# Performance work log

Measured on AMD Instinct MI355X. Metric: run time of the kernel, lower is better.

## Reference

```python
import jax, jax.numpy as jnp
import numpy as np

N1 = 64          # n1 (rows of matching matrix)
N2 = 64          # n2 (cols); N = n1*n2 association-graph nodes
N = N1 * N2
DENSITY = 0.15   # sparsity of affinity matrix K
CH = [64, 64, 64]
TAU = 0.05
SK_ITERS = 20


def _sinkhorn(s):
    # log-domain Sinkhorn, tau=0.05, 20 alternating row/col normalizations.
    # n1 == n2 here, so the dummy_row padding in the original is a no-op.
    log_s = s / TAU
    for i in range(SK_ITERS):
        log_s = log_s - jax.nn.logsumexp(log_s, axis=(1 if i % 2 == 0 else 0), keepdims=True)
    return jnp.exp(log_s)


def _lin(k, i, o, scale=0.1):
    kw, kb = jax.random.split(k)
    return (jax.random.normal(kw, (i, o), jnp.float32) * scale,
            jax.random.normal(kb, (o,), jnp.float32) * scale)


def setup_inputs() -> dict:
    key = jax.random.key(0)
    ks = jax.random.split(key, 16)
    mask = jax.random.uniform(ks[0], (N, N)) < DENSITY
    mask = mask | jnp.eye(N, dtype=bool)          # diag(K) supplies node features
    K = jnp.where(mask, jax.random.normal(ks[1], (N, N), jnp.float32), 0.0)
    # identical to torch: (K != 0).nonzero(as_tuple=False).t()
    edge_index = jnp.stack(jnp.nonzero(K)).astype(jnp.int32)
    inp = {"K": K, "edge_index": edge_index, "n1": N1, "n2": N2}
    dims_in = [1, CH[0], CH[1]]
    ki = 2
    for l in range(3):
        cw, cb = _lin(ks[ki], dims_in[l], CH[l]); ki += 1
        sw, sb = _lin(ks[ki], dims_in[l], CH[l]); ki += 1
        kw, kb = _lin(ks[ki], CH[l], 1); ki += 1
        inp.update({f"conv_w{l}": cw, f"conv_b{l}": cb,
                    f"self_w{l}": sw, f"self_b{l}": sb,
                    f"cls_w{l}": kw, f"cls_b{l}": kb})
    fw, fb = _lin(ks[ki], CH[2], 1)
    inp["fin_w"] = fw
    inp["fin_b"] = fb
    return inp


def _forward(K, edge_index, n1, n2, layer_params, fin_w, fin_b):
    n_nodes = n1 * n2
    src, dst = edge_index[0], edge_index[1]
    loop = jnp.arange(n_nodes, dtype=src.dtype)
    # PyG gcn_norm / add_remaining_self_loops: existing self-loop edges get
    # weight replaced (zeroed here, re-added with weight 1 below).
    w = jnp.concatenate([(src != dst).astype(K.dtype), jnp.ones((n_nodes,), K.dtype)])
    src_f = jnp.concatenate([src, loop])
    dst_f = jnp.concatenate([dst, loop])
    deg = jax.ops.segment_sum(w, dst_f, num_segments=n_nodes)
    dis = jnp.where(deg > 0, jax.lax.rsqrt(deg), 0.0)
    norm = dis[src_f] * w * dis[dst_f]                    # (E+N,)

    x = jnp.diag(K)[:, None]                              # (N, 1) node features
    for (cw, cb, sw, sb, kw, kb) in layer_params:
        xw = x @ cw                                       # (N, out)
        x_neigh = jax.ops.segment_sum(norm[:, None] * xw[src_f], dst_f,
                                      num_segments=n_nodes) + cb
        x_out = (x @ sw + sb) + x_neigh                   # self-loop + GCNConv
        sk = _sinkhorn((x_out @ kw + kb).reshape(n1, n2))
        x = x_out + sk.reshape(n_nodes, 1)                # broadcast over channels
    scores = x @ fin_w + fin_b                            # (N, 1)
    s = scores.reshape(n2, n1).T                          # (n1, n2)
    return _sinkhorn(s)


def reference(K, edge_index, n1, n2,
              conv_w0, conv_b0, self_w0, self_b0, cls_w0, cls_b0,
              conv_w1, conv_b1, self_w1, self_b1, cls_w1, cls_b1,
              conv_w2, conv_b2, self_w2, self_b2, cls_w2, cls_b2,
              fin_w, fin_b):
    layer_params = [(conv_w0, conv_b0, self_w0, self_b0, cls_w0, cls_b0),
                    (conv_w1, conv_b1, self_w1, self_b1, cls_w1, cls_b1),
                    (conv_w2, conv_b2, self_w2, self_b2, cls_w2, cls_b2)]
    return _forward(K, edge_index, n1, n2, layer_params, fin_w, fin_b)
```

## Files before the change

kernel.cpp:

```cpp
#include <hip/hip_runtime.h>
#include <hip/hip_bf16.h>
#include <cstdint>
#include <cstddef>

#define NN 4096

typedef float f32x4 __attribute__((ext_vector_type(4)));
typedef short s16x8 __attribute__((ext_vector_type(8)));

__global__ __launch_bounds__(256) void k_prep(const float* __restrict__ K,
                                              unsigned long long* __restrict__ maskT) {
  const int lane = threadIdx.x & 63;
  const int wv = threadIdx.x >> 6;
  const int d0 = blockIdx.x * 256 + lane * 4;
  const int sbase = blockIdx.y * 256 + wv * 64;
  const int chunk = blockIdx.y * 4 + wv;
  unsigned long long w0 = 0, w1 = 0, w2 = 0, w3 = 0;
#pragma unroll 8
  for (int i = 0; i < 64; ++i) {
    const float4 kv = *(const float4*)(K + (size_t)(sbase + i) * NN + d0);
    w0 |= ((unsigned long long)(kv.x != 0.0f)) << i;
    w1 |= ((unsigned long long)(kv.y != 0.0f)) << i;
    w2 |= ((unsigned long long)(kv.z != 0.0f)) << i;
    w3 |= ((unsigned long long)(kv.w != 0.0f)) << i;
  }
  unsigned long long* mp = maskT + (size_t)chunk * NN + d0;
  mp[0] = w0; mp[1] = w1; mp[2] = w2; mp[3] = w3;
}

__device__ __forceinline__ void sinkhorn_pots(const float* __restrict__ matR,
    const float* __restrict__ matC, float* __restrict__ potU, float* __restrict__ potV,
    float* __restrict__ pp, int tid) {
  const int l = tid & 63;
  const int w = tid >> 6;
  const int jb = w * 16;
  if (w == 0) potV[l] = 0.f;
  __syncthreads();
  for (int it = 0; it < 20; ++it) {
    const bool row = (it & 1) == 0;
    const float* src = row ? matR : matC;
    const float* pot = row ? potV : potU;
    f32x4 x0 = *(const f32x4*)&src[l * 68 + jb];
    f32x4 x1 = *(const f32x4*)&src[l * 68 + jb + 4];
    f32x4 x2 = *(const f32x4*)&src[l * 68 + jb + 8];
    f32x4 x3 = *(const f32x4*)&src[l * 68 + jb + 12];
    const f32x4 p0 = *(const f32x4*)&pot[jb];
    const f32x4 p1 = *(const f32x4*)&pot[jb + 4];
    const f32x4 p2 = *(const f32x4*)&pot[jb + 8];
    const f32x4 p3 = *(const f32x4*)&pot[jb + 12];
    x0 -= p0; x1 -= p1; x2 -= p2; x3 -= p3;
    f32x4 mA;
#pragma unroll
    for (int i = 0; i < 4; ++i)
      mA[i] = fmaxf(fmaxf(x0[i], x1[i]), fmaxf(x2[i], x3[i]));
    const float mx = fmaxf(fmaxf(mA[0], mA[1]), fmaxf(mA[2], mA[3]));
    float sm = 0.f;
#pragma unroll
    for (int i = 0; i < 4; ++i)
      sm += __expf(x0[i] - mx) + __expf(x1[i] - mx) +
            __expf(x2[i] - mx) + __expf(x3[i] - mx);
    pp[l * 12 + w] = mx;
    pp[l * 12 + 4 + w] = sm;
    __syncthreads();
    if (w == 0) {
      const f32x4 pm = *(const f32x4*)&pp[l * 12];
      const f32x4 ps = *(const f32x4*)&pp[l * 12 + 4];
      const float mM = fmaxf(fmaxf(pm[0], pm[1]), fmaxf(pm[2], pm[3]));
      const float ss = ps[0] * __expf(pm[0] - mM) + ps[1] * __expf(pm[1] - mM)
                     + ps[2] * __expf(pm[2] - mM) + ps[3] * __expf(pm[3] - mM);
      const float lse = mM + __logf(ss);
      (row ? potU : potV)[l] = lse;
    }
    __syncthreads();
  }
}

__global__ __launch_bounds__(256) void k_xform0(const float* __restrict__ K,
    const unsigned long long* __restrict__ maskT,
    const float* __restrict__ cw, const float* __restrict__ cb,
    const float* __restrict__ sw, const float* __restrict__ sb,
    float* __restrict__ disv,
    __hip_bfloat16* __restrict__ gHi, __hip_bfloat16* __restrict__ gLo,
    float* __restrict__ xselfT) {
  __shared__ float pdeg[4][64];
  const int lane = threadIdx.x & 63;
  const int wv = threadIdx.x >> 6;
  const int s = blockIdx.x * 64 + lane;
  unsigned cnt = 0;
#pragma unroll
  for (int q = 0; q < 16; ++q)
    cnt += (unsigned)__popcll(maskT[(size_t)(wv * 16 + q) * NN + s]);
  pdeg[wv][lane] = (float)cnt;
  __syncthreads();
  const float ds = rsqrtf(pdeg[0][lane] + pdeg[1][lane] + pdeg[2][lane] + pdeg[3][lane]);
  if (wv == 0) disv[s] = ds;
  const float xv = K[(size_t)s * NN + s];
#pragma unroll
  for (int i = 0; i < 16; ++i) {
    const int c = wv * 16 + i;
    const float gv = ds * xv * cw[c];
    const __hip_bfloat16 hi = __float2bfloat16(gv);
    gHi[(size_t)c * NN + s] = hi;
    gLo[(size_t)c * NN + s] = __float2bfloat16(gv - __bfloat162float(hi));
    xselfT[(size_t)c * NN + s] = xv * sw[c] + sb[c] + cb[c];
  }
}

__global__ __launch_bounds__(256, 1) void k_xform(const float* __restrict__ v,
    const float* __restrict__ vT,
    const float* __restrict__ xoutT, const float* __restrict__ disv,
    const float* __restrict__ cw, const float* __restrict__ cb,
    const float* __restrict__ sw, const float* __restrict__ sb,
    __hip_bfloat16* __restrict__ gHi, __hip_bfloat16* __restrict__ gLo,
    float* __restrict__ xselfT) {
  __shared__ __align__(16) float matR[64 * 68];
  __shared__ __align__(16) float matC[64 * 68];
  __shared__ float xt[64][64];
  __shared__ float wcl[64 * 32], wsl[64 * 32];
  __shared__ __align__(16) float potU[64], potV[64], pp[64 * 12];
  const int tid = threadIdx.x;
  const int l = tid & 63;
  const int w = tid >> 6;
  const int jb = w * 16;
  const int s = blockIdx.x * 64 + l;
  const int cbase = blockIdx.y * 32;
#pragma unroll
  for (int q = 0; q < 4; ++q) {
    *(f32x4*)&matR[l * 68 + jb + 4 * q] = *(const f32x4*)&v[l * 64 + jb + 4 * q] * 20.0f;
    *(f32x4*)&matC[l * 68 + jb + 4 * q] = *(const f32x4*)&vT[l * 64 + jb + 4 * q] * 20.0f;
  }
#pragma unroll
  for (int r = 0; r < 16; ++r)
    xt[w * 16 + r][l] = xoutT[(size_t)(w * 16 + r) * NN + s];
#pragma unroll
  for (int q = 0; q < 8; ++q) {
    const int e = w * 512 + q * 64 + l;
    const int k = e >> 5, cl = e & 31;
    wcl[e] = cw[k * 64 + cbase + cl];
    wsl[e] = sw[k * 64 + cbase + cl];
  }
  sinkhorn_pots(matR, matC, potU, potV, pp, tid);
  const int cl0 = w * 8;
  float accC[8], accS[8], csum[8], ssum[8];
#pragma unroll
  for (int i = 0; i < 8; ++i) { accC[i] = 0.f; accS[i] = 0.f; csum[i] = 0.f; ssum[i] = 0.f; }
  for (int k = 0; k < 64; ++k) {
    const float xv = xt[k][l];
    const f32x4 wcA = *(const f32x4*)&wcl[k * 32 + cl0];
    const f32x4 wcB = *(const f32x4*)&wcl[k * 32 + cl0 + 4];
    const f32x4 wsA = *(const f32x4*)&wsl[k * 32 + cl0];
    const f32x4 wsB = *(const f32x4*)&wsl[k * 32 + cl0 + 4];
#pragma unroll
    for (int i = 0; i < 4; ++i) {
      accC[i]     = fmaf(xv, wcA[i], accC[i]);     csum[i]     += wcA[i];
      accC[i + 4] = fmaf(xv, wcB[i], accC[i + 4]); csum[i + 4] += wcB[i];
      accS[i]     = fmaf(xv, wsA[i], accS[i]);     ssum[i]     += wsA[i];
      accS[i + 4] = fmaf(xv, wsB[i], accS[i + 4]); ssum[i + 4] += wsB[i];
    }
  }
  const float skv = __expf(matR[blockIdx.x * 68 + l] - potU[blockIdx.x] - potV[l]);
  const float ds = disv[s];
#pragma unroll
  for (int i = 0; i < 8; ++i) {
    const int c = cbase + cl0 + i;
    const float gv = ds * (accC[i] + skv * csum[i]);
    const __hip_bfloat16 hi = __float2bfloat16(gv);
    gHi[(size_t)c * NN + s] = hi;
    gLo[(size_t)c * NN + s] = __float2bfloat16(gv - __bfloat162float(hi));
    xselfT[(size_t)c * NN + s] = accS[i] + skv * ssum[i] + sb[c] + cb[c];
  }
}

__global__ __launch_bounds__(512) void k_agg(const unsigned long long* __restrict__ maskT,
    const __hip_bfloat16* __restrict__ gHi, const __hip_bfloat16* __restrict__ gLo,
    const float* __restrict__ xselfT, const float* __restrict__ disv,
    const float* __restrict__ kw, const float* __restrict__ kb,
    const float* __restrict__ fw, const float* __restrict__ fb,
    float* __restrict__ xoutT, float* __restrict__ v, float* __restrict__ vT,
    float* __restrict__ sbF) {
  const int tid = threadIdx.x;
  const int lane = tid & 63;
  const int wv = tid >> 6;
  const int mtile = wv & 3;
  const int ks = wv >> 2;
  const int l15 = lane & 15;
  const int h = lane >> 4;
  const int d = blockIdx.x * 16 + l15;
  const int ch = mtile * 16 + l15;
  const short* __restrict__ gh = (const short*)gHi;
  const short* __restrict__ gl = (const short*)gLo;
  f32x4 acch = {0.f, 0.f, 0.f, 0.f};
  f32x4 accl = {0.f, 0.f, 0.f, 0.f};
  const int c0 = ks * 32;
#pragma unroll 4
  for (int c = c0; c < c0 + 32; ++c) {
    const unsigned long long w = maskT[(size_t)c * NN + d];
    const unsigned half0 = (unsigned)w, half1 = (unsigned)(w >> 32);
#pragma unroll
    for (int t = 0; t < 2; ++t) {
      const unsigned half = t ? half1 : half0;
      const unsigned hb = (half >> (8 * h)) & 0xFFu;
      s16x8 bfr;
#pragma unroll
      for (int j = 0; j < 8; ++j)
        bfr[j] = (short)(((hb >> j) & 1u) * 0x3F80u);
      const size_t abase = (size_t)ch * NN + (size_t)(c * 64 + t * 32 + 8 * h);
      const s16x8 ah = *(const s16x8*)(gh + abase);
      const s16x8 al = *(const s16x8*)(gl + abase);
      acch = __builtin_amdgcn_mfma_f32_16x16x32_bf16(ah, bfr, acch, 0, 0, 0);
      accl = __builtin_amdgcn_mfma_f32_16x16x32_bf16(al, bfr, accl, 0, 0, 0);
    }
  }
  __shared__ float rbuf[4][64][5];
  __shared__ float vred[16][17];
  __shared__ float vred2[16][17];
  f32x4 tot;
#pragma unroll
  for (int r = 0; r < 4; ++r) tot[r] = acch[r] + accl[r];
  if (ks == 1) {
#pragma unroll
    for (int r = 0; r < 4; ++r) rbuf[mtile][lane][r] = tot[r];
  }
  __syncthreads();
  if (ks == 0) {
    const float dd = disv[d];
    float p = 0.f, p2 = 0.f;
#pragma unroll
    for (int r = 0; r < 4; ++r) {
      const int chr = mtile * 16 + h * 4 + r;
      const float xo = xselfT[(size_t)chr * NN + d] + dd * (tot[r] + rbuf[mtile][lane][r]);
      xoutT[(size_t)chr * NN + d] = xo;
      p = fmaf(xo, kw[chr], p);
      p2 = fmaf(xo, fw[chr], p2);
    }
    vred[l15][mtile * 4 + h] = p;
    vred2[l15][mtile * 4 + h] = p2;
  }
  __syncthreads();
  if (tid < 16) {
    float sum = kb[0];
#pragma unroll
    for (int q = 0; q < 16; ++q) sum += vred[tid][q];
    const int d2 = blockIdx.x * 16 + tid;
    v[d2] = sum;
    vT[(d2 & 63) * 64 + (d2 >> 6)] = sum;
    if (sbF != nullptr) {
      float sum2 = fb[0];
#pragma unroll
      for (int q = 0; q < 16; ++q) sum2 += vred2[tid][q];
      sbF[d2] = sum2;
    }
  }
}

__global__ __launch_bounds__(256, 1) void k_final(const float* __restrict__ v,
    const float* __restrict__ vT, const float* __restrict__ sbF,
    const float* __restrict__ fw, float* __restrict__ out) {
  __shared__ __align__(16) float matR[64 * 68];
  __shared__ __align__(16) float matC[64 * 68];
  __shared__ __align__(16) float scR[64 * 68];
  __shared__ __align__(16) float scT[64 * 68];
  __shared__ float scfl[NN];
  __shared__ float fwl[64];
  __shared__ __align__(16) float potU[64], potV[64], pp[64 * 12];
  const int tid = threadIdx.x;
  const int l = tid & 63;
  const int w = tid >> 6;
  const int jb = w * 16;
#pragma unroll
  for (int q = 0; q < 4; ++q) {
    *(f32x4*)&matR[l * 68 + jb + 4 * q] = *(const f32x4*)&v[l * 64 + jb + 4 * q] * 20.0f;
    *(f32x4*)&matC[l * 68 + jb + 4 * q] = *(const f32x4*)&vT[l * 64 + jb + 4 * q] * 20.0f;
  }
#pragma unroll
  for (int q = 0; q < 4; ++q) {
    const int n0 = q * 1024 + tid * 4;
    *(f32x4*)&scfl[n0] = *(const f32x4*)&sbF[n0];
  }
  if (tid < 64) fwl[tid] = fw[tid];
  sinkhorn_pots(matR, matC, potU, potV, pp, tid);
  float sumw = 0.f;
#pragma unroll
  for (int k = 0; k < 64; ++k) sumw += fwl[k];
#pragma unroll
  for (int k = 0; k < 16; ++k) {
    const int n = k * 256 + tid;
    const int r2 = 4 * k + w;
    const float sk2 = __expf(matR[r2 * 68 + l] - potU[r2] - potV[l]);
    const float val = (scfl[n] + sk2 * sumw) * 20.0f;
    scR[l * 68 + r2] = val;
    scT[r2 * 68 + l] = val;
  }
  __syncthreads();
  sinkhorn_pots(scR, scT, potU, potV, pp, tid);
#pragma unroll
  for (int q = 0; q < 16; ++q) {
    const int e = q * 256 + tid;
    const int i1 = 4 * q + w;
    out[e] = __expf(scR[i1 * 68 + l] - potU[i1] - potV[l]);
  }
}

extern "C" void kernel_launch(void* const* d_in, const int* in_sizes, int n_in,
                              void* d_out, int out_size, void* d_ws, size_t ws_size,
                              hipStream_t stream) {
  const float* K = (const float*)d_in[0];
  const float* cw[3] = {(const float*)d_in[4],  (const float*)d_in[10], (const float*)d_in[16]};
  const float* cb[3] = {(const float*)d_in[5],  (const float*)d_in[11], (const float*)d_in[17]};
  const float* sw[3] = {(const float*)d_in[6],  (const float*)d_in[12], (const float*)d_in[18]};
  const float* sb[3] = {(const float*)d_in[7],  (const float*)d_in[13], (const float*)d_in[19]};
  const float* kw[3] = {(const float*)d_in[8],  (const float*)d_in[14], (const float*)d_in[20]};
  const float* kb[3] = {(const float*)d_in[9],  (const float*)d_in[15], (const float*)d_in[21]};
  const float* fw = (const float*)d_in[22];
  const float* fb = (const float*)d_in[23];
  float* out = (float*)d_out;

  char* ws = (char*)d_ws;
  const size_t KB = 1024, MB = 1024 * 1024;
  float* disv               = (float*)(ws + 0);
  float* v                  = (float*)(ws + 16 * KB);
  float* vT                 = (float*)(ws + 32 * KB);
  float* sbF                = (float*)(ws + 48 * KB);
  unsigned long long* maskT = (unsigned long long*)(ws + 64 * KB);
  __hip_bfloat16* gHi       = (__hip_bfloat16*)(ws + 64 * KB + 2 * MB);
  __hip_bfloat16* gLo       = (__hip_bfloat16*)(ws + 64 * KB + 2 * MB + 512 * KB);
  float* xselfT             = (float*)(ws + 64 * KB + 3 * MB);
  float* xoutT              = (float*)(ws + 64 * KB + 4 * MB);
  (void)in_sizes; (void)n_in; (void)out_size; (void)ws_size;

  k_prep<<<dim3(16, 16), 256, 0, stream>>>(K, maskT);
  k_xform0<<<64, 256, 0, stream>>>(K, maskT, cw[0], cb[0], sw[0], sb[0],
                                   disv, gHi, gLo, xselfT);
  k_agg<<<256, 512, 0, stream>>>(maskT, gHi, gLo, xselfT, disv, kw[0], kb[0],
                                 fw, fb, xoutT, v, vT, nullptr);
  for (int l = 1; l < 3; ++l) {
    k_xform<<<dim3(64, 2), 256, 0, stream>>>(v, vT, xoutT, disv, cw[l], cb[l], sw[l], sb[l],
                                             gHi, gLo, xselfT);
    k_agg<<<256, 512, 0, stream>>>(maskT, gHi, gLo, xselfT, disv, kw[l], kb[l],
                                   fw, fb, xoutT, v, vT, (l == 2) ? sbF : nullptr);
  }
  k_final<<<1, 256, 0, stream>>>(v, vT, sbF, fw, out);
}
```

Before: 188.4 us.

## Keep Sinkhorn matrix and potentials in registers with a single barrier per iteration

Rewrites the Sinkhorn potential loop so each thread keeps its 16 matrix elements in registers. Potentials are broadcast with readlane instead of being read from shared memory. Every wave now computes the row/column log-sum-exp redundantly, and a double-buffered partial array lets each iteration get by with one barrier instead of two. The cost is more registers and duplicated reduction work across waves, in kernels that run on very few blocks.

```diff
diff --git a/kernel.cpp b/kernel.cpp
--- a/kernel.cpp
+++ b/kernel.cpp
@@ -7,6 +7,10 @@
 
 typedef float f32x4 __attribute__((ext_vector_type(4)));
 typedef short s16x8 __attribute__((ext_vector_type(8)));
+
+__device__ __forceinline__ float rdlane(float x, int lane) {
+  return __int_as_float(__builtin_amdgcn_readlane(__float_as_int(x), lane));
+}
 
 __global__ __launch_bounds__(256) void k_prep(const float* __restrict__ K,
                                               unsigned long long* __restrict__ maskT) {
@@ -28,50 +32,41 @@
   mp[0] = w0; mp[1] = w1; mp[2] = w2; mp[3] = w3;
 }
 
-__device__ __forceinline__ void sinkhorn_pots(const float* __restrict__ matR,
-    const float* __restrict__ matC, float* __restrict__ potU, float* __restrict__ potV,
-    float* __restrict__ pp, int tid) {
-  const int l = tid & 63;
-  const int w = tid >> 6;
-  const int jb = w * 16;
-  if (w == 0) potV[l] = 0.f;
-  __syncthreads();
+__device__ __forceinline__ void sinkhorn_reg(const float (&xR)[16], const float (&xC)[16],
+    float& U, float& V, float* __restrict__ pp, int l, int w, int jb) {
+  U = 0.f; V = 0.f;
+#pragma unroll
   for (int it = 0; it < 20; ++it) {
     const bool row = (it & 1) == 0;
-    const float* src = row ? matR : matC;
-    const float* pot = row ? potV : potU;
-    f32x4 x0 = *(const f32x4*)&src[l * 68 + jb];
-    f32x4 x1 = *(const f32x4*)&src[l * 68 + jb + 4];
-    f32x4 x2 = *(const f32x4*)&src[l * 68 + jb + 8];
-    f32x4 x3 = *(const f32x4*)&src[l * 68 + jb + 12];
-    const f32x4 p0 = *(const f32x4*)&pot[jb];
-    const f32x4 p1 = *(const f32x4*)&pot[jb + 4];
-    const f32x4 p2 = *(const f32x4*)&pot[jb + 8];
-    const f32x4 p3 = *(const f32x4*)&pot[jb + 12];
-    x0 -= p0; x1 -= p1; x2 -= p2; x3 -= p3;
-    f32x4 mA;
-#pragma unroll
-    for (int i = 0; i < 4; ++i)
-      mA[i] = fmaxf(fmaxf(x0[i], x1[i]), fmaxf(x2[i], x3[i]));
-    const float mx = fmaxf(fmaxf(mA[0], mA[1]), fmaxf(mA[2], mA[3]));
-    float sm = 0.f;
-#pragma unroll
-    for (int i = 0; i < 4; ++i)
-      sm += __expf(x0[i] - mx) + __expf(x1[i] - mx) +
-            __expf(x2[i] - mx) + __expf(x3[i] - mx);
-    pp[l * 12 + w] = mx;
-    pp[l * 12 + 4 + w] = sm;
+    float t[16];
+#pragma unroll
+    for (int j = 0; j < 16; ++j) {
+      const float pot = rdlane(row ? V : U, jb + j);
+      t[j] = (row ? xR[j] : xC[j]) - pot;
+    }
+    float a0 = fmaxf(t[0], t[1]),  a1 = fmaxf(t[2], t[3]);
+    float a2 = fmaxf(t[4], t[5]),  a3 = fmaxf(t[6], t[7]);
+    a0 = fmaxf(a0, fmaxf(t[8], t[9]));   a1 = fmaxf(a1, fmaxf(t[10], t[11]));
+    a2 = fmaxf(a2, fmaxf(t[12], t[13])); a3 = fmaxf(a3, fmaxf(t[14], t[15]));
+    const float mx = fmaxf(fmaxf(a0, a1), fmaxf(a2, a3));
+    float s0 = 0.f, s1 = 0.f, s2 = 0.f, s3 = 0.f;
+#pragma unroll
+    for (int j = 0; j < 16; j += 4) {
+      s0 += __expf(t[j] - mx);     s1 += __expf(t[j + 1] - mx);
+      s2 += __expf(t[j + 2] - mx); s3 += __expf(t[j + 3] - mx);
+    }
+    const float sm = (s0 + s1) + (s2 + s3);
+    float* buf = pp + (it & 1) * 768;
+    buf[l * 12 + w] = mx;
+    buf[l * 12 + 4 + w] = sm;
     __syncthreads();
-    if (w == 0) {
-      const f32x4 pm = *(const f32x4*)&pp[l * 12];
-      const f32x4 ps = *(const f32x4*)&pp[l * 12 + 4];
-      const float mM = fmaxf(fmaxf(pm[0], pm[1]), fmaxf(pm[2], pm[3]));
-      const float ss = ps[0] * __expf(pm[0] - mM) + ps[1] * __expf(pm[1] - mM)
-                     + ps[2] * __expf(pm[2] - mM) + ps[3] * __expf(pm[3] - mM);
-      const float lse = mM + __logf(ss);
-      (row ? potU : potV)[l] = lse;
-    }
-    __syncthreads();
+    const f32x4 pm = *(const f32x4*)&buf[l * 12];
+    const f32x4 ps = *(const f32x4*)&buf[l * 12 + 4];
+    const float mM = fmaxf(fmaxf(pm[0], pm[1]), fmaxf(pm[2], pm[3]));
+    const float ss = ps[0] * __expf(pm[0] - mM) + ps[1] * __expf(pm[1] - mM)
+                   + ps[2] * __expf(pm[2] - mM) + ps[3] * __expf(pm[3] - mM);
+    const float lse = mM + __logf(ss);
+    if (row) U = lse; else V = lse;
   }
 }
 
@@ -113,21 +108,20 @@
     const float* __restrict__ sw, const float* __restrict__ sb,
     __hip_bfloat16* __restrict__ gHi, __hip_bfloat16* __restrict__ gLo,
     float* __restrict__ xselfT) {
-  __shared__ __align__(16) float matR[64 * 68];
-  __shared__ __align__(16) float matC[64 * 68];
+  __shared__ __align__(16) float pp[2 * 768];
   __shared__ float xt[64][64];
   __shared__ float wcl[64 * 32], wsl[64 * 32];
-  __shared__ __align__(16) float potU[64], potV[64], pp[64 * 12];
   const int tid = threadIdx.x;
   const int l = tid & 63;
   const int w = tid >> 6;
   const int jb = w * 16;
   const int s = blockIdx.x * 64 + l;
   const int cbase = blockIdx.y * 32;
+  float xR[16], xC[16];
 #pragma unroll
   for (int q = 0; q < 4; ++q) {
-    *(f32x4*)&matR[l * 68 + jb + 4 * q] = *(const f32x4*)&v[l * 64 + jb + 4 * q] * 20.0f;
-    *(f32x4*)&matC[l * 68 + jb + 4 * q] = *(const f32x4*)&vT[l * 64 + jb + 4 * q] * 20.0f;
+    *(f32x4*)&xR[4 * q] = *(const f32x4*)&v[l * 64 + jb + 4 * q] * 20.0f;
+    *(f32x4*)&xC[4 * q] = *(const f32x4*)&vT[l * 64 + jb + 4 * q] * 20.0f;
   }
 #pragma unroll
   for (int r = 0; r < 16; ++r)
@@ -139,7 +133,8 @@
     wcl[e] = cw[k * 64 + cbase + cl];
     wsl[e] = sw[k * 64 + cbase + cl];
   }
-  sinkhorn_pots(matR, matC, potU, potV, pp, tid);
+  float U, V;
+  sinkhorn_reg(xR, xC, U, V, pp, l, w, jb);
   const int cl0 = w * 8;
   float accC[8], accS[8], csum[8], ssum[8];
 #pragma unroll
@@ -158,7 +153,8 @@
       accS[i + 4] = fmaf(xv, wsB[i], accS[i + 4]); ssum[i + 4] += wsB[i];
     }
   }
-  const float skv = __expf(matR[blockIdx.x * 68 + l] - potU[blockIdx.x] - potV[l]);
+  const int bx = blockIdx.x;
+  const float skv = __expf(20.0f * v[bx * 64 + l] - rdlane(U, bx) - V);
   const float ds = disv[s];
 #pragma unroll
   for (int i = 0; i < 8; ++i) {
@@ -256,29 +252,23 @@
 __global__ __launch_bounds__(256, 1) void k_final(const float* __restrict__ v,
     const float* __restrict__ vT, const float* __restrict__ sbF,
     const float* __restrict__ fw, float* __restrict__ out) {
-  __shared__ __align__(16) float matR[64 * 68];
-  __shared__ __align__(16) float matC[64 * 68];
+  __shared__ __align__(16) float pp[2 * 768];
   __shared__ __align__(16) float scR[64 * 68];
   __shared__ __align__(16) float scT[64 * 68];
-  __shared__ float scfl[NN];
   __shared__ float fwl[64];
-  __shared__ __align__(16) float potU[64], potV[64], pp[64 * 12];
   const int tid = threadIdx.x;
   const int l = tid & 63;
   const int w = tid >> 6;
   const int jb = w * 16;
+  float xR[16], xC[16];
 #pragma unroll
   for (int q = 0; q < 4; ++q) {
-    *(f32x4*)&matR[l * 68 + jb + 4 * q] = *(const f32x4*)&v[l * 64 + jb + 4 * q] * 20.0f;
-    *(f32x4*)&matC[l * 68 + jb + 4 * q] = *(const f32x4*)&vT[l * 64 + jb + 4 * q] * 20.0f;
-  }
-#pragma unroll
-  for (int q = 0; q < 4; ++q) {
-    const int n0 = q * 1024 + tid * 4;
-    *(f32x4*)&scfl[n0] = *(const f32x4*)&sbF[n0];
+    *(f32x4*)&xR[4 * q] = *(const f32x4*)&v[l * 64 + jb + 4 * q] * 20.0f;
+    *(f32x4*)&xC[4 * q] = *(const f32x4*)&vT[l * 64 + jb + 4 * q] * 20.0f;
   }
   if (tid < 64) fwl[tid] = fw[tid];
-  sinkhorn_pots(matR, matC, potU, potV, pp, tid);
+  float U1, V1;
+  sinkhorn_reg(xR, xC, U1, V1, pp, l, w, jb);
   float sumw = 0.f;
 #pragma unroll
   for (int k = 0; k < 64; ++k) sumw += fwl[k];
@@ -286,18 +276,24 @@
   for (int k = 0; k < 16; ++k) {
     const int n = k * 256 + tid;
     const int r2 = 4 * k + w;
-    const float sk2 = __expf(matR[r2 * 68 + l] - potU[r2] - potV[l]);
-    const float val = (scfl[n] + sk2 * sumw) * 20.0f;
+    const float sk2 = __expf(20.0f * v[n] - rdlane(U1, r2) - V1);
+    const float val = (sbF[n] + sk2 * sumw) * 20.0f;
     scR[l * 68 + r2] = val;
     scT[r2 * 68 + l] = val;
   }
   __syncthreads();
-  sinkhorn_pots(scR, scT, potU, potV, pp, tid);
+#pragma unroll
+  for (int q = 0; q < 4; ++q) {
+    *(f32x4*)&xR[4 * q] = *(const f32x4*)&scR[l * 68 + jb + 4 * q];
+    *(f32x4*)&xC[4 * q] = *(const f32x4*)&scT[l * 68 + jb + 4 * q];
+  }
+  float U2, V2;
+  sinkhorn_reg(xR, xC, U2, V2, pp, l, w, jb);
 #pragma unroll
   for (int q = 0; q < 16; ++q) {
     const int e = q * 256 + tid;
     const int i1 = 4 * q + w;
-    out[e] = __expf(scR[i1 * 68 + l] - potU[i1] - potV[l]);
+    out[e] = __expf(scR[i1 * 68 + l] - rdlane(U2, i1) - V2);
   }
 }
 
```

New measurement: 197.7 us. +4.9%, slower.
